# Kernel tuning notes

Hardware: AMD Instinct MI355X
Metric: run time of the kernel (lower is better)

## Reference

```python
import jax, jax.numpy as jnp
import numpy as np

N_NODES = 50000
N_EDGES = 800000
NFEAT, NHID, NCLASS = 512, 64, 40


def setup_inputs() -> dict:
    key = jax.random.key(0)
    ks = jax.random.split(key, 8)
    x = jax.random.normal(ks[0], (N_NODES, NFEAT), dtype=jnp.float32)
    adj_vals = jax.random.uniform(ks[1], (N_EDGES,), dtype=jnp.float32)
    W1 = jax.random.normal(ks[2], (NFEAT, NHID), dtype=jnp.float32) / np.sqrt(NFEAT)
    b1 = jax.random.normal(ks[3], (NHID,), dtype=jnp.float32) * 0.01
    W2 = jax.random.normal(ks[4], (NHID, NCLASS), dtype=jnp.float32) / np.sqrt(NHID)
    b2 = jax.random.normal(ks[5], (NCLASS,), dtype=jnp.float32) * 0.01
    src = jax.random.randint(ks[6], (N_EDGES,), 0, N_NODES, dtype=jnp.int32)
    dst = jax.random.randint(ks[7], (N_EDGES,), 0, N_NODES, dtype=jnp.int32)
    return {"x": x, "adj_vals": adj_vals, "W1": W1, "b1": b1,
            "W2": W2, "b2": b2, "src": src, "dst": dst}


def reference(x, adj_vals, W1, b1, W2, b2, src, dst):
    # GCN forward (quant=False, eval mode => dropout is identity):
    #   h   = relu(adj @ (x @ W1) + b1)
    #   out = adj @ (h @ W2) + b2
    #   return log_softmax(out, dim=1)
    # adj is sparse COO: out[dst] += vals * feats[src]
    n = x.shape[0]

    def spmm(feats):  # [N, d] -> [N, d]
        msgs = adj_vals[:, None] * feats[src]          # [E, d] gather + scale
        return jax.ops.segment_sum(msgs, dst, num_segments=n)

    h = jax.nn.relu(spmm(x @ W1) + b1)                 # [N, nhid]
    out = spmm(h @ W2) + b2                            # [N, nclass]
    return jax.nn.log_softmax(out, axis=1)
```

## Files before the change

kernel.cpp:

```cpp
#include <hip/hip_runtime.h>
#include <math.h>

#define N_NODES 50000
#define N_EDGES 800000
#define NFEAT   512
#define NHID    64
#define NCLASS  40
#define SLOTS   64

#define GEMM_BLOCKS ((N_NODES + 63) / 64)
#define SCAT_BLOCKS (N_EDGES / 256)

typedef __attribute__((ext_vector_type(8))) short bf16x8;
typedef __attribute__((ext_vector_type(4))) float f32x4;

__device__ inline unsigned short f2bf(float f) {
    unsigned int u = __float_as_uint(f);
    u += 0x7FFFu + ((u >> 16) & 1u);
    return (unsigned short)(u >> 16);
}
__device__ inline float bf2f(unsigned short u) {
    return __uint_as_float(((unsigned int)u) << 16);
}


__global__ void init_kernel(int* __restrict__ cursor,
                            const float* __restrict__ W1,
                            unsigned short* __restrict__ w1t) {
    int i = blockIdx.x * blockDim.x + threadIdx.x;
    if (i < N_NODES) cursor[i] = 0;
    if (i < NFEAT * NHID) {
        int k = i >> 6, c = i & 63;
        w1t[(size_t)c * NFEAT + k] = f2bf(W1[i]);
    }
}

__global__ __launch_bounds__(256) void gemm1_scatter_kernel(
        const float* __restrict__ x,
        const unsigned short* __restrict__ w1t,
        unsigned short* __restrict__ xw,
        const int* __restrict__ dst,
        const int* __restrict__ src,
        const float* __restrict__ adj_vals,
        int* __restrict__ cursor,
        unsigned int* __restrict__ ev2) {
    const int tid = threadIdx.x;
    const unsigned b = blockIdx.x;

    if (b >= GEMM_BLOCKS) {
        const int i = (b - GEMM_BLOCKS) * 256 + tid;
        const int d = dst[i];
        const int p = atomicAdd(&cursor[d], 1);
        if (p < SLOTS)
            ev2[(size_t)d * SLOTS + p] =
                (unsigned int)src[i] | ((unsigned int)f2bf(adj_vals[i]) << 16);
        return;
    }

    const int lane = tid & 63;
    const int wv   = tid >> 6;
    const int i16  = lane & 15;
    const int quad = lane >> 4;

    const int arow = b * 64 + wv * 16 + i16;
    const int arc  = arow < N_NODES ? arow : N_NODES - 1;
    const float* xrow = x + (size_t)arc * NFEAT + quad * 8;
    const unsigned short* wb = w1t + (size_t)i16 * NFEAT + quad * 8;

    f32x4 acc0 = {0.f, 0.f, 0.f, 0.f};
    f32x4 acc1 = acc0, acc2 = acc0, acc3 = acc0;

    float4 pa[4], pb[4];
    bf16x8 bf0[2], bf1[2], bf2[2], bf3[2];

#pragma unroll
    for (int s = 0; s < 4; ++s) {
        pa[s] = *reinterpret_cast<const float4*>(xrow + s * 32);
        pb[s] = *reinterpret_cast<const float4*>(xrow + s * 32 + 4);
    }
#pragma unroll
    for (int s = 0; s < 2; ++s) {
        bf0[s] = *reinterpret_cast<const bf16x8*>(wb + 0 * 16 * NFEAT + s * 32);
        bf1[s] = *reinterpret_cast<const bf16x8*>(wb + 1 * 16 * NFEAT + s * 32);
        bf2[s] = *reinterpret_cast<const bf16x8*>(wb + 2 * 16 * NFEAT + s * 32);
        bf3[s] = *reinterpret_cast<const bf16x8*>(wb + 3 * 16 * NFEAT + s * 32);
    }

#pragma unroll
    for (int s = 0; s < 16; ++s) {
        float4 xa = pa[s & 3], xb = pb[s & 3];
        bf16x8 a;
        a[0] = (short)f2bf(xa.x); a[1] = (short)f2bf(xa.y);
        a[2] = (short)f2bf(xa.z); a[3] = (short)f2bf(xa.w);
        a[4] = (short)f2bf(xb.x); a[5] = (short)f2bf(xb.y);
        a[6] = (short)f2bf(xb.z); a[7] = (short)f2bf(xb.w);
        acc0 = __builtin_amdgcn_mfma_f32_16x16x32_bf16(a, bf0[s & 1], acc0, 0, 0, 0);
        acc1 = __builtin_amdgcn_mfma_f32_16x16x32_bf16(a, bf1[s & 1], acc1, 0, 0, 0);
        acc2 = __builtin_amdgcn_mfma_f32_16x16x32_bf16(a, bf2[s & 1], acc2, 0, 0, 0);
        acc3 = __builtin_amdgcn_mfma_f32_16x16x32_bf16(a, bf3[s & 1], acc3, 0, 0, 0);
        if (s + 4 < 16) {
            pa[s & 3] = *reinterpret_cast<const float4*>(xrow + (s + 4) * 32);
            pb[s & 3] = *reinterpret_cast<const float4*>(xrow + (s + 4) * 32 + 4);
        }
        if (s + 2 < 16) {
            bf0[s & 1] = *reinterpret_cast<const bf16x8*>(wb + 0 * 16 * NFEAT + (s + 2) * 32);
            bf1[s & 1] = *reinterpret_cast<const bf16x8*>(wb + 1 * 16 * NFEAT + (s + 2) * 32);
            bf2[s & 1] = *reinterpret_cast<const bf16x8*>(wb + 2 * 16 * NFEAT + (s + 2) * 32);
            bf3[s & 1] = *reinterpret_cast<const bf16x8*>(wb + 3 * 16 * NFEAT + (s + 2) * 32);
        }
    }

    const int orow0 = b * 64 + wv * 16 + quad * 4;
#pragma unroll
    for (int reg = 0; reg < 4; ++reg) {
        const int orow = orow0 + reg;
        if (orow < N_NODES) {
            unsigned short* op = xw + (size_t)orow * NHID + i16;
            op[ 0] = f2bf(acc0[reg]);
            op[16] = f2bf(acc1[reg]);
            op[32] = f2bf(acc2[reg]);
            op[48] = f2bf(acc3[reg]);
        }
    }
}

__global__ __launch_bounds__(256) void spmm1_gemm2_kernel(
        const unsigned short* __restrict__ xw,
        const unsigned int* __restrict__ ev2,
        const int* __restrict__ counts,
        const float* __restrict__ b1,
        const float* __restrict__ W2,
        unsigned short* __restrict__ hw) {
    __shared__ float w2lds[NHID * NCLASS];
    __shared__ float hlds[4][NHID];
    const int tid  = threadIdx.x;
    const int lane = tid & 63;
    const int wv   = tid >> 6;

    for (int idx = tid; idx < NHID * NCLASS; idx += 256) w2lds[idx] = W2[idx];
    __syncthreads();

    const int row = blockIdx.x * 4 + wv;
    int cnt = counts[row];
    if (cnt > SLOTS) cnt = SLOTS;
    const unsigned int* erow = ev2 + (size_t)row * SLOTS;

    float acc = 0.f;
    int i = 0;
    for (; i + 7 < cnt; i += 8) {
        unsigned int e[8];
#pragma unroll
        for (int j = 0; j < 8; ++j) e[j] = erow[i + j];
        unsigned short g[8];
#pragma unroll
        for (int j = 0; j < 8; ++j)
            g[j] = xw[(size_t)(e[j] & 0xFFFFu) * NHID + lane];
#pragma unroll
        for (int j = 0; j < 8; ++j)
            acc += __uint_as_float(e[j] & 0xFFFF0000u) * bf2f(g[j]);
    }
    for (; i < cnt; ++i) {
        unsigned int e = erow[i];
        acc += __uint_as_float(e & 0xFFFF0000u) * bf2f(xw[(size_t)(e & 0xFFFFu) * NHID + lane]);
    }

    hlds[wv][lane] = fmaxf(acc + b1[lane], 0.f);

    if (lane < 20) {
        const int c0 = lane * 2;
        float d0 = 0.f, d1 = 0.f;
#pragma unroll
        for (int k = 0; k < NHID; ++k) {
            float hv = hlds[wv][k];
            d0 = fmaf(hv, w2lds[k * NCLASS + c0],     d0);
            d1 = fmaf(hv, w2lds[k * NCLASS + c0 + 1], d1);
        }
        unsigned int pack = (unsigned int)f2bf(d0) | ((unsigned int)f2bf(d1) << 16);
        *reinterpret_cast<unsigned int*>(hw + (size_t)row * 64 + c0) = pack;
    }
}

__global__ void spmm2_lsm_kernel(const unsigned short* __restrict__ hw,
                                 const unsigned int* __restrict__ ev2,
                                 const int* __restrict__ counts,
                                 const float* __restrict__ b2,
                                 float* __restrict__ out) {
    const int lane = threadIdx.x & 63;
    const int row  = blockIdx.x * 4 + (threadIdx.x >> 6);
    const bool active = lane < NCLASS;
    const int cl = active ? lane : (NCLASS - 1);
    int cnt = counts[row];
    if (cnt > SLOTS) cnt = SLOTS;
    const unsigned int* erow = ev2 + (size_t)row * SLOTS;
    float acc = 0.f;
    int i = 0;
    for (; i + 7 < cnt; i += 8) {
        unsigned int e[8];
#pragma unroll
        for (int j = 0; j < 8; ++j) e[j] = erow[i + j];
        unsigned short g[8];
#pragma unroll
        for (int j = 0; j < 8; ++j)
            g[j] = hw[(size_t)(e[j] & 0xFFFFu) * 64 + cl];
#pragma unroll
        for (int j = 0; j < 8; ++j)
            acc += __uint_as_float(e[j] & 0xFFFF0000u) * bf2f(g[j]);
    }
    for (; i < cnt; ++i) {
        unsigned int e = erow[i];
        acc += __uint_as_float(e & 0xFFFF0000u) * bf2f(hw[(size_t)(e & 0xFFFFu) * 64 + cl]);
    }

    float logit = acc + b2[cl];
    float m = active ? logit : -INFINITY;
#pragma unroll
    for (int o = 32; o > 0; o >>= 1) m = fmaxf(m, __shfl_xor(m, o));
    float ex = active ? expf(logit - m) : 0.f;
    float ssum = ex;
#pragma unroll
    for (int o = 32; o > 0; o >>= 1) ssum += __shfl_xor(ssum, o);
    if (active) out[(size_t)row * NCLASS + lane] = logit - m - logf(ssum);
}


extern "C" void kernel_launch(void* const* d_in, const int* in_sizes, int n_in,
                              void* d_out, int out_size, void* d_ws, size_t ws_size,
                              hipStream_t stream) {
    const float* x        = (const float*)d_in[0];
    const float* adj_vals = (const float*)d_in[1];
    const float* W1       = (const float*)d_in[2];
    const float* b1       = (const float*)d_in[3];
    const float* W2       = (const float*)d_in[4];
    const float* b2       = (const float*)d_in[5];
    const int*   src      = (const int*)d_in[6];
    const int*   dst      = (const int*)d_in[7];
    float* out = (float*)d_out;

    const size_t OFF_HW   = 6400000;
    const size_t OFF_CUR  = 12800000;
    const size_t OFF_EV   = 13000000;
    const size_t REQUIRED = OFF_EV + (size_t)N_NODES * SLOTS * 4;
    if (ws_size < REQUIRED) return;

    char* ws = (char*)d_ws;
    unsigned short* xw     = (unsigned short*)(ws);
    unsigned short* hw     = (unsigned short*)(ws + OFF_HW);
    unsigned short* w1t    = (unsigned short*)(ws + OFF_HW);
    int*            cursor = (int*)  (ws + OFF_CUR);
    unsigned int*   ev2    = (unsigned int*)(ws + OFF_EV);

    init_kernel<<<(N_NODES + 255) / 256, 256, 0, stream>>>(cursor, W1, w1t);
    gemm1_scatter_kernel<<<GEMM_BLOCKS + SCAT_BLOCKS, 256, 0, stream>>>(
        x, w1t, xw, dst, src, adj_vals, cursor, ev2);
    spmm1_gemm2_kernel<<<N_NODES / 4, 256, 0, stream>>>(xw, ev2, cursor, b1, W2, hw);
    spmm2_lsm_kernel<<<N_NODES / 4, 256, 0, stream>>>(hw, ev2, cursor, b2, out);
}
```

Measured before the change: 312.7 us.

## Retile GEMM1 to 16-row blocks and interleave with edge-scatter blocks

The first GEMM now gives each block 16 node rows, with each of the four waves computing one 16-column slice of the 64 hidden outputs. Before, each wave computed all four column tiles for its own 16 rows. Block indices alternate between GEMM and scatter work (odd blocks scatter edges), so the atomic bucket-fill runs alongside the bandwidth-bound x reads. This gives more and smaller blocks and better mixing of the two kinds of work. In exchange, all four waves of a block reload the same x rows, which depends on cache hits, and the row-bounds guard is gone because N_NODES divides evenly by 16.

```diff
diff --git a/kernel.cpp b/kernel.cpp
--- a/kernel.cpp
+++ b/kernel.cpp
@@ -8,7 +8,7 @@
 #define NCLASS  40
 #define SLOTS   64
 
-#define GEMM_BLOCKS ((N_NODES + 63) / 64)
+#define GEMM_BLOCKS (N_NODES / 16)
 #define SCAT_BLOCKS (N_EDGES / 256)
 
 typedef __attribute__((ext_vector_type(8))) short bf16x8;
@@ -47,8 +47,8 @@
     const int tid = threadIdx.x;
     const unsigned b = blockIdx.x;
 
-    if (b >= GEMM_BLOCKS) {
-        const int i = (b - GEMM_BLOCKS) * 256 + tid;
+    if (b & 1u) {
+        const int i = (b >> 1) * 256 + tid;
         const int d = dst[i];
         const int p = atomicAdd(&cursor[d], 1);
         if (p < SLOTS)
@@ -57,21 +57,19 @@
         return;
     }
 
+    const int gb   = b >> 1;
     const int lane = tid & 63;
     const int wv   = tid >> 6;
     const int i16  = lane & 15;
     const int quad = lane >> 4;
 
-    const int arow = b * 64 + wv * 16 + i16;
-    const int arc  = arow < N_NODES ? arow : N_NODES - 1;
-    const float* xrow = x + (size_t)arc * NFEAT + quad * 8;
-    const unsigned short* wb = w1t + (size_t)i16 * NFEAT + quad * 8;
-
-    f32x4 acc0 = {0.f, 0.f, 0.f, 0.f};
-    f32x4 acc1 = acc0, acc2 = acc0, acc3 = acc0;
+    const float* xrow = x + (size_t)(gb * 16 + i16) * NFEAT + quad * 8;
+    const unsigned short* wb = w1t + (size_t)(wv * 16 + i16) * NFEAT + quad * 8;
+
+    f32x4 acc = {0.f, 0.f, 0.f, 0.f};
 
     float4 pa[4], pb[4];
-    bf16x8 bf0[2], bf1[2], bf2[2], bf3[2];
+    bf16x8 bf[2];
 
 #pragma unroll
     for (int s = 0; s < 4; ++s) {
@@ -79,12 +77,8 @@
         pb[s] = *reinterpret_cast<const float4*>(xrow + s * 32 + 4);
     }
 #pragma unroll
-    for (int s = 0; s < 2; ++s) {
-        bf0[s] = *reinterpret_cast<const bf16x8*>(wb + 0 * 16 * NFEAT + s * 32);
-        bf1[s] = *reinterpret_cast<const bf16x8*>(wb + 1 * 16 * NFEAT + s * 32);
-        bf2[s] = *reinterpret_cast<const bf16x8*>(wb + 2 * 16 * NFEAT + s * 32);
-        bf3[s] = *reinterpret_cast<const bf16x8*>(wb + 3 * 16 * NFEAT + s * 32);
-    }
+    for (int s = 0; s < 2; ++s)
+        bf[s] = *reinterpret_cast<const bf16x8*>(wb + s * 32);
 
 #pragma unroll
     for (int s = 0; s < 16; ++s) {
@@ -94,34 +88,19 @@
         a[2] = (short)f2bf(xa.z); a[3] = (short)f2bf(xa.w);
         a[4] = (short)f2bf(xb.x); a[5] = (short)f2bf(xb.y);
         a[6] = (short)f2bf(xb.z); a[7] = (short)f2bf(xb.w);
-        acc0 = __builtin_amdgcn_mfma_f32_16x16x32_bf16(a, bf0[s & 1], acc0, 0, 0, 0);
-        acc1 = __builtin_amdgcn_mfma_f32_16x16x32_bf16(a, bf1[s & 1], acc1, 0, 0, 0);
-        acc2 = __builtin_amdgcn_mfma_f32_16x16x32_bf16(a, bf2[s & 1], acc2, 0, 0, 0);
-        acc3 = __builtin_amdgcn_mfma_f32_16x16x32_bf16(a, bf3[s & 1], acc3, 0, 0, 0);
+        acc = __builtin_amdgcn_mfma_f32_16x16x32_bf16(a, bf[s & 1], acc, 0, 0, 0);
         if (s + 4 < 16) {
             pa[s & 3] = *reinterpret_cast<const float4*>(xrow + (s + 4) * 32);
             pb[s & 3] = *reinterpret_cast<const float4*>(xrow + (s + 4) * 32 + 4);
         }
-        if (s + 2 < 16) {
-            bf0[s & 1] = *reinterpret_cast<const bf16x8*>(wb + 0 * 16 * NFEAT + (s + 2) * 32);
-            bf1[s & 1] = *reinterpret_cast<const bf16x8*>(wb + 1 * 16 * NFEAT + (s + 2) * 32);
-            bf2[s & 1] = *reinterpret_cast<const bf16x8*>(wb + 2 * 16 * NFEAT + (s + 2) * 32);
-            bf3[s & 1] = *reinterpret_cast<const bf16x8*>(wb + 3 * 16 * NFEAT + (s + 2) * 32);
-        }
-    }
-
-    const int orow0 = b * 64 + wv * 16 + quad * 4;
-#pragma unroll
-    for (int reg = 0; reg < 4; ++reg) {
-        const int orow = orow0 + reg;
-        if (orow < N_NODES) {
-            unsigned short* op = xw + (size_t)orow * NHID + i16;
-            op[ 0] = f2bf(acc0[reg]);
-            op[16] = f2bf(acc1[reg]);
-            op[32] = f2bf(acc2[reg]);
-            op[48] = f2bf(acc3[reg]);
-        }
-    }
+        if (s + 2 < 16)
+            bf[s & 1] = *reinterpret_cast<const bf16x8*>(wb + (s + 2) * 32);
+    }
+
+    unsigned short* op = xw + (size_t)(gb * 16 + quad * 4) * NHID + wv * 16 + i16;
+#pragma unroll
+    for (int reg = 0; reg < 4; ++reg)
+        op[(size_t)reg * NHID] = f2bf(acc[reg]);
 }
 
 __global__ __launch_bounds__(256) void spmm1_gemm2_kernel(
```

After: 382.7 us. 1.22x slower.

## Zero-pad edge slots to drop SpMM tail loops; add nontemporal loads/stores

Applied to the files above, without the earlier changes.

The init kernel now zeroes the whole per-node edge-slot buffer (3125 blocks x 256 threads x 16 bytes), so unused slots hold zero weights. Both SpMM kernels can then always process edges in full groups of 8 and drop the scalar remainder loop. The x loads in the GEMM and the scattered edge stores now use nontemporal hints to limit cache pollution. In exchange, the init kernel writes an extra 12.8 MB to memory and the SpMM loops may gather up to 7 padding entries per row, which read node 0's features with zero weight.

```diff
diff --git a/kernel.cpp b/kernel.cpp
--- a/kernel.cpp
+++ b/kernel.cpp
@@ -24,15 +24,17 @@
 }
 
 
-__global__ void init_kernel(int* __restrict__ cursor,
-                            const float* __restrict__ W1,
-                            unsigned short* __restrict__ w1t) {
+__global__ __launch_bounds__(256) void init_kernel(int* __restrict__ cursor,
+                                                   const float* __restrict__ W1,
+                                                   unsigned short* __restrict__ w1t,
+                                                   uint4* __restrict__ ev2q) {
     int i = blockIdx.x * blockDim.x + threadIdx.x;
     if (i < N_NODES) cursor[i] = 0;
     if (i < NFEAT * NHID) {
         int k = i >> 6, c = i & 63;
         w1t[(size_t)c * NFEAT + k] = f2bf(W1[i]);
     }
+    ev2q[i] = make_uint4(0u, 0u, 0u, 0u);
 }
 
 __global__ __launch_bounds__(256) void gemm1_scatter_kernel(
@@ -52,8 +54,9 @@
         const int d = dst[i];
         const int p = atomicAdd(&cursor[d], 1);
         if (p < SLOTS)
-            ev2[(size_t)d * SLOTS + p] =
-                (unsigned int)src[i] | ((unsigned int)f2bf(adj_vals[i]) << 16);
+            __builtin_nontemporal_store(
+                (unsigned int)src[i] | ((unsigned int)f2bf(adj_vals[i]) << 16),
+                &ev2[(size_t)d * SLOTS + p]);
         return;
     }
 
@@ -70,13 +73,13 @@
     f32x4 acc0 = {0.f, 0.f, 0.f, 0.f};
     f32x4 acc1 = acc0, acc2 = acc0, acc3 = acc0;
 
-    float4 pa[4], pb[4];
+    f32x4 pa[4], pb[4];
     bf16x8 bf0[2], bf1[2], bf2[2], bf3[2];
 
 #pragma unroll
     for (int s = 0; s < 4; ++s) {
-        pa[s] = *reinterpret_cast<const float4*>(xrow + s * 32);
-        pb[s] = *reinterpret_cast<const float4*>(xrow + s * 32 + 4);
+        pa[s] = __builtin_nontemporal_load(reinterpret_cast<const f32x4*>(xrow + s * 32));
+        pb[s] = __builtin_nontemporal_load(reinterpret_cast<const f32x4*>(xrow + s * 32 + 4));
     }
 #pragma unroll
     for (int s = 0; s < 2; ++s) {
@@ -88,19 +91,21 @@
 
 #pragma unroll
     for (int s = 0; s < 16; ++s) {
-        float4 xa = pa[s & 3], xb = pb[s & 3];
+        f32x4 xa = pa[s & 3], xb = pb[s & 3];
         bf16x8 a;
-        a[0] = (short)f2bf(xa.x); a[1] = (short)f2bf(xa.y);
-        a[2] = (short)f2bf(xa.z); a[3] = (short)f2bf(xa.w);
-        a[4] = (short)f2bf(xb.x); a[5] = (short)f2bf(xb.y);
-        a[6] = (short)f2bf(xb.z); a[7] = (short)f2bf(xb.w);
+        a[0] = (short)f2bf(xa[0]); a[1] = (short)f2bf(xa[1]);
+        a[2] = (short)f2bf(xa[2]); a[3] = (short)f2bf(xa[3]);
+        a[4] = (short)f2bf(xb[0]); a[5] = (short)f2bf(xb[1]);
+        a[6] = (short)f2bf(xb[2]); a[7] = (short)f2bf(xb[3]);
         acc0 = __builtin_amdgcn_mfma_f32_16x16x32_bf16(a, bf0[s & 1], acc0, 0, 0, 0);
         acc1 = __builtin_amdgcn_mfma_f32_16x16x32_bf16(a, bf1[s & 1], acc1, 0, 0, 0);
         acc2 = __builtin_amdgcn_mfma_f32_16x16x32_bf16(a, bf2[s & 1], acc2, 0, 0, 0);
         acc3 = __builtin_amdgcn_mfma_f32_16x16x32_bf16(a, bf3[s & 1], acc3, 0, 0, 0);
         if (s + 4 < 16) {
-            pa[s & 3] = *reinterpret_cast<const float4*>(xrow + (s + 4) * 32);
-            pb[s & 3] = *reinterpret_cast<const float4*>(xrow + (s + 4) * 32 + 4);
+            pa[s & 3] = __builtin_nontemporal_load(
+                reinterpret_cast<const f32x4*>(xrow + (s + 4) * 32));
+            pb[s & 3] = __builtin_nontemporal_load(
+                reinterpret_cast<const f32x4*>(xrow + (s + 4) * 32 + 4));
         }
         if (s + 2 < 16) {
             bf0[s & 1] = *reinterpret_cast<const bf16x8*>(wb + 0 * 16 * NFEAT + (s + 2) * 32);
@@ -146,8 +151,7 @@
     const unsigned int* erow = ev2 + (size_t)row * SLOTS;
 
     float acc = 0.f;
-    int i = 0;
-    for (; i + 7 < cnt; i += 8) {
+    for (int i = 0; i < cnt; i += 8) {
         unsigned int e[8];
 #pragma unroll
         for (int j = 0; j < 8; ++j) e[j] = erow[i + j];
@@ -158,10 +162,6 @@
 #pragma unroll
         for (int j = 0; j < 8; ++j)
             acc += __uint_as_float(e[j] & 0xFFFF0000u) * bf2f(g[j]);
-    }
-    for (; i < cnt; ++i) {
-        unsigned int e = erow[i];
-        acc += __uint_as_float(e & 0xFFFF0000u) * bf2f(xw[(size_t)(e & 0xFFFFu) * NHID + lane]);
     }
 
     hlds[wv][lane] = fmaxf(acc + b1[lane], 0.f);
@@ -192,9 +192,9 @@
     int cnt = counts[row];
     if (cnt > SLOTS) cnt = SLOTS;
     const unsigned int* erow = ev2 + (size_t)row * SLOTS;
+
     float acc = 0.f;
-    int i = 0;
-    for (; i + 7 < cnt; i += 8) {
+    for (int i = 0; i < cnt; i += 8) {
         unsigned int e[8];
 #pragma unroll
         for (int j = 0; j < 8; ++j) e[j] = erow[i + j];
@@ -205,10 +205,6 @@
 #pragma unroll
         for (int j = 0; j < 8; ++j)
             acc += __uint_as_float(e[j] & 0xFFFF0000u) * bf2f(g[j]);
-    }
-    for (; i < cnt; ++i) {
-        unsigned int e = erow[i];
-        acc += __uint_as_float(e & 0xFFFF0000u) * bf2f(hw[(size_t)(e & 0xFFFFu) * 64 + cl]);
     }
 
     float logit = acc + b2[cl];
@@ -249,7 +245,7 @@
     int*            cursor = (int*)  (ws + OFF_CUR);
     unsigned int*   ev2    = (unsigned int*)(ws + OFF_EV);
 
-    init_kernel<<<(N_NODES + 255) / 256, 256, 0, stream>>>(cursor, W1, w1t);
+    init_kernel<<<3125, 256, 0, stream>>>(cursor, W1, w1t, (uint4*)ev2);
     gemm1_scatter_kernel<<<GEMM_BLOCKS + SCAT_BLOCKS, 256, 0, stream>>>(
         x, w1t, xw, dst, src, adj_vals, cursor, ev2);
     spmm1_gemm2_kernel<<<N_NODES / 4, 256, 0, stream>>>(xw, ev2, cursor, b1, W2, hw);
```

Result: no change. 310.4 us (-0.7%).

## Vectorize SpMM gathers with 4-wide bf16 loads across edge-parallel lane groups

Applied to the files above, without the earlier changes.

Both SpMM kernels now split each wavefront into four edge groups of 16 lanes. Each lane gathers four bf16 features with one 8-byte load and accumulates four outputs, and the groups are combined with cross-lane shuffles. The aim is fewer, wider memory transactions per gathered row and more independent loads in flight. Reading past the edge count needs zero padding, so the whole edge-slot buffer is zeroed in init, which adds about 12.8MB of writes. The padding columns of hw are zeroed as well. Log-softmax is restructured so each lane handles four classes.

```diff
diff --git a/kernel.cpp b/kernel.cpp
--- a/kernel.cpp
+++ b/kernel.cpp
@@ -22,17 +22,25 @@
 __device__ inline float bf2f(unsigned short u) {
     return __uint_as_float(((unsigned int)u) << 16);
 }
-
-
-__global__ void init_kernel(int* __restrict__ cursor,
-                            const float* __restrict__ W1,
-                            unsigned short* __restrict__ w1t) {
+__device__ inline float bflo(unsigned int u) {
+    return __uint_as_float(u << 16);
+}
+__device__ inline float bfhi(unsigned int u) {
+    return __uint_as_float(u & 0xFFFF0000u);
+}
+
+
+__global__ __launch_bounds__(256) void init_kernel(int* __restrict__ cursor,
+                                                   const float* __restrict__ W1,
+                                                   unsigned short* __restrict__ w1t,
+                                                   uint4* __restrict__ ev2q) {
     int i = blockIdx.x * blockDim.x + threadIdx.x;
     if (i < N_NODES) cursor[i] = 0;
     if (i < NFEAT * NHID) {
         int k = i >> 6, c = i & 63;
         w1t[(size_t)c * NFEAT + k] = f2bf(W1[i]);
     }
+    ev2q[i] = make_uint4(0u, 0u, 0u, 0u);
 }
 
 __global__ __launch_bounds__(256) void gemm1_scatter_kernel(
@@ -136,6 +144,8 @@
     const int tid  = threadIdx.x;
     const int lane = tid & 63;
     const int wv   = tid >> 6;
+    const int ep   = lane >> 4;
+    const int f    = lane & 15;
 
     for (int idx = tid; idx < NHID * NCLASS; idx += 256) w2lds[idx] = W2[idx];
     __syncthreads();
@@ -145,26 +155,40 @@
     if (cnt > SLOTS) cnt = SLOTS;
     const unsigned int* erow = ev2 + (size_t)row * SLOTS;
 
-    float acc = 0.f;
-    int i = 0;
-    for (; i + 7 < cnt; i += 8) {
-        unsigned int e[8];
-#pragma unroll
-        for (int j = 0; j < 8; ++j) e[j] = erow[i + j];
-        unsigned short g[8];
-#pragma unroll
-        for (int j = 0; j < 8; ++j)
-            g[j] = xw[(size_t)(e[j] & 0xFFFFu) * NHID + lane];
-#pragma unroll
-        for (int j = 0; j < 8; ++j)
-            acc += __uint_as_float(e[j] & 0xFFFF0000u) * bf2f(g[j]);
-    }
-    for (; i < cnt; ++i) {
-        unsigned int e = erow[i];
-        acc += __uint_as_float(e & 0xFFFF0000u) * bf2f(xw[(size_t)(e & 0xFFFFu) * NHID + lane]);
-    }
-
-    hlds[wv][lane] = fmaxf(acc + b1[lane], 0.f);
+    float a0 = 0.f, a1 = 0.f, a2 = 0.f, a3 = 0.f;
+    for (int i = ep; i < cnt; i += 16) {
+        unsigned int e0 = erow[i];
+        unsigned int e1 = erow[i + 4];
+        unsigned int e2 = erow[i + 8];
+        unsigned int e3 = erow[i + 12];
+        uint2 g0 = *reinterpret_cast<const uint2*>(xw + (size_t)(e0 & 0xFFFFu) * NHID + f * 4);
+        uint2 g1 = *reinterpret_cast<const uint2*>(xw + (size_t)(e1 & 0xFFFFu) * NHID + f * 4);
+        uint2 g2 = *reinterpret_cast<const uint2*>(xw + (size_t)(e2 & 0xFFFFu) * NHID + f * 4);
+        uint2 g3 = *reinterpret_cast<const uint2*>(xw + (size_t)(e3 & 0xFFFFu) * NHID + f * 4);
+        float v0 = bfhi(e0), v1 = bfhi(e1), v2 = bfhi(e2), v3 = bfhi(e3);
+        a0 = fmaf(v0, bflo(g0.x), a0); a1 = fmaf(v0, bfhi(g0.x), a1);
+        a2 = fmaf(v0, bflo(g0.y), a2); a3 = fmaf(v0, bfhi(g0.y), a3);
+        a0 = fmaf(v1, bflo(g1.x), a0); a1 = fmaf(v1, bfhi(g1.x), a1);
+        a2 = fmaf(v1, bflo(g1.y), a2); a3 = fmaf(v1, bfhi(g1.y), a3);
+        a0 = fmaf(v2, bflo(g2.x), a0); a1 = fmaf(v2, bfhi(g2.x), a1);
+        a2 = fmaf(v2, bflo(g2.y), a2); a3 = fmaf(v2, bfhi(g2.y), a3);
+        a0 = fmaf(v3, bflo(g3.x), a0); a1 = fmaf(v3, bfhi(g3.x), a1);
+        a2 = fmaf(v3, bflo(g3.y), a2); a3 = fmaf(v3, bfhi(g3.y), a3);
+    }
+    a0 += __shfl_xor(a0, 16); a0 += __shfl_xor(a0, 32);
+    a1 += __shfl_xor(a1, 16); a1 += __shfl_xor(a1, 32);
+    a2 += __shfl_xor(a2, 16); a2 += __shfl_xor(a2, 32);
+    a3 += __shfl_xor(a3, 16); a3 += __shfl_xor(a3, 32);
+
+    if (ep == 0) {
+        float4 bv = *reinterpret_cast<const float4*>(b1 + f * 4);
+        float4 hv;
+        hv.x = fmaxf(a0 + bv.x, 0.f);
+        hv.y = fmaxf(a1 + bv.y, 0.f);
+        hv.z = fmaxf(a2 + bv.z, 0.f);
+        hv.w = fmaxf(a3 + bv.w, 0.f);
+        *reinterpret_cast<float4*>(&hlds[wv][f * 4]) = hv;
+    }
 
     if (lane < 20) {
         const int c0 = lane * 2;
@@ -177,6 +201,8 @@
         }
         unsigned int pack = (unsigned int)f2bf(d0) | ((unsigned int)f2bf(d1) << 16);
         *reinterpret_cast<unsigned int*>(hw + (size_t)row * 64 + c0) = pack;
+    } else if (lane < 32) {
+        *reinterpret_cast<unsigned int*>(hw + (size_t)row * 64 + lane * 2) = 0u;
     }
 }
 
@@ -187,39 +213,55 @@
                                  float* __restrict__ out) {
     const int lane = threadIdx.x & 63;
     const int row  = blockIdx.x * 4 + (threadIdx.x >> 6);
-    const bool active = lane < NCLASS;
-    const int cl = active ? lane : (NCLASS - 1);
+    const int ep   = lane >> 4;
+    const int f    = lane & 15;
     int cnt = counts[row];
     if (cnt > SLOTS) cnt = SLOTS;
     const unsigned int* erow = ev2 + (size_t)row * SLOTS;
-    float acc = 0.f;
-    int i = 0;
-    for (; i + 7 < cnt; i += 8) {
-        unsigned int e[8];
-#pragma unroll
-        for (int j = 0; j < 8; ++j) e[j] = erow[i + j];
-        unsigned short g[8];
-#pragma unroll
-        for (int j = 0; j < 8; ++j)
-            g[j] = hw[(size_t)(e[j] & 0xFFFFu) * 64 + cl];
-#pragma unroll
-        for (int j = 0; j < 8; ++j)
-            acc += __uint_as_float(e[j] & 0xFFFF0000u) * bf2f(g[j]);
-    }
-    for (; i < cnt; ++i) {
-        unsigned int e = erow[i];
-        acc += __uint_as_float(e & 0xFFFF0000u) * bf2f(hw[(size_t)(e & 0xFFFFu) * 64 + cl]);
-    }
-
-    float logit = acc + b2[cl];
-    float m = active ? logit : -INFINITY;
-#pragma unroll
-    for (int o = 32; o > 0; o >>= 1) m = fmaxf(m, __shfl_xor(m, o));
-    float ex = active ? expf(logit - m) : 0.f;
-    float ssum = ex;
-#pragma unroll
-    for (int o = 32; o > 0; o >>= 1) ssum += __shfl_xor(ssum, o);
-    if (active) out[(size_t)row * NCLASS + lane] = logit - m - logf(ssum);
+
+    float a0 = 0.f, a1 = 0.f, a2 = 0.f, a3 = 0.f;
+    for (int i = ep; i < cnt; i += 16) {
+        unsigned int e0 = erow[i];
+        unsigned int e1 = erow[i + 4];
+        unsigned int e2 = erow[i + 8];
+        unsigned int e3 = erow[i + 12];
+        uint2 g0 = *reinterpret_cast<const uint2*>(hw + (size_t)(e0 & 0xFFFFu) * 64 + f * 4);
+        uint2 g1 = *reinterpret_cast<const uint2*>(hw + (size_t)(e1 & 0xFFFFu) * 64 + f * 4);
+        uint2 g2 = *reinterpret_cast<const uint2*>(hw + (size_t)(e2 & 0xFFFFu) * 64 + f * 4);
+        uint2 g3 = *reinterpret_cast<const uint2*>(hw + (size_t)(e3 & 0xFFFFu) * 64 + f * 4);
+        float v0 = bfhi(e0), v1 = bfhi(e1), v2 = bfhi(e2), v3 = bfhi(e3);
+        a0 = fmaf(v0, bflo(g0.x), a0); a1 = fmaf(v0, bfhi(g0.x), a1);
+        a2 = fmaf(v0, bflo(g0.y), a2); a3 = fmaf(v0, bfhi(g0.y), a3);
+        a0 = fmaf(v1, bflo(g1.x), a0); a1 = fmaf(v1, bfhi(g1.x), a1);
+        a2 = fmaf(v1, bflo(g1.y), a2); a3 = fmaf(v1, bfhi(g1.y), a3);
+        a0 = fmaf(v2, bflo(g2.x), a0); a1 = fmaf(v2, bfhi(g2.x), a1);
+        a2 = fmaf(v2, bflo(g2.y), a2); a3 = fmaf(v2, bfhi(g2.y), a3);
+        a0 = fmaf(v3, bflo(g3.x), a0); a1 = fmaf(v3, bfhi(g3.x), a1);
+        a2 = fmaf(v3, bflo(g3.y), a2); a3 = fmaf(v3, bfhi(g3.y), a3);
+    }
+    a0 += __shfl_xor(a0, 16); a0 += __shfl_xor(a0, 32);
+    a1 += __shfl_xor(a1, 16); a1 += __shfl_xor(a1, 32);
+    a2 += __shfl_xor(a2, 16); a2 += __shfl_xor(a2, 32);
+    a3 += __shfl_xor(a3, 16); a3 += __shfl_xor(a3, 32);
+
+    const bool active = f < 10;
+    const int  fb     = active ? f : 9;
+    float4 bv = *reinterpret_cast<const float4*>(b2 + fb * 4);
+    float l0 = a0 + bv.x, l1 = a1 + bv.y, l2 = a2 + bv.z, l3 = a3 + bv.w;
+
+    float m = active ? fmaxf(fmaxf(l0, l1), fmaxf(l2, l3)) : -INFINITY;
+#pragma unroll
+    for (int o = 8; o > 0; o >>= 1) m = fmaxf(m, __shfl_xor(m, o));
+    float s = active ? (expf(l0 - m) + expf(l1 - m) + expf(l2 - m) + expf(l3 - m)) : 0.f;
+#pragma unroll
+    for (int o = 8; o > 0; o >>= 1) s += __shfl_xor(s, o);
+    const float lse = m + logf(s);
+
+    if (active && ep == 0) {
+        float4 o4;
+        o4.x = l0 - lse; o4.y = l1 - lse; o4.z = l2 - lse; o4.w = l3 - lse;
+        *reinterpret_cast<float4*>(&out[(size_t)row * NCLASS + f * 4]) = o4;
+    }
 }
 
 
@@ -249,7 +291,7 @@
     int*            cursor = (int*)  (ws + OFF_CUR);
     unsigned int*   ev2    = (unsigned int*)(ws + OFF_EV);
 
-    init_kernel<<<(N_NODES + 255) / 256, 256, 0, stream>>>(cursor, W1, w1t);
+    init_kernel<<<3125, 256, 0, stream>>>(cursor, W1, w1t, (uint4*)ev2);
     gemm1_scatter_kernel<<<GEMM_BLOCKS + SCAT_BLOCKS, 256, 0, stream>>>(
         x, w1t, xw, dst, src, adj_vals, cursor, ev2);
     spmm1_gemm2_kernel<<<N_NODES / 4, 256, 0, stream>>>(xw, ev2, cursor, b1, W2, hw);
```

New measurement: 287.7 us. 1.09x faster.
